# Kernel optimization log

Hardware: AMD Instinct MI355X
Metric: run time of the kernel (lower is better)

Reference implementation:

```python
import jax, jax.numpy as jnp
import numpy as np

B, T, D_FEAT, FREQ, HID = 256, 128, 128, 16, 128


def setup_inputs() -> dict:
    key = jax.random.key(0)
    ks = jax.random.split(key, 14)
    n = lambda k, s, sc: jax.random.normal(k, s, jnp.float32) * sc
    sx = float(np.sqrt(2.0 / (D_FEAT + HID)))   # xavier-ish for W_*
    sf = float(np.sqrt(2.0 / (D_FEAT + FREQ)))
    sh = float(np.sqrt(1.0 / HID))              # stand-in for orthogonal U_*
    return {
        "input": jax.random.normal(ks[0], (B, D_FEAT * T), jnp.float32),
        "W_i": n(ks[1], (D_FEAT, HID), sx), "U_i": n(ks[2], (HID, HID), sh), "b_i": jnp.zeros((HID,), jnp.float32),
        "W_ste": n(ks[3], (D_FEAT, HID), sx), "U_ste": n(ks[4], (HID, HID), sh), "b_ste": jnp.ones((HID,), jnp.float32),
        "W_fre": n(ks[5], (D_FEAT, FREQ), sf), "U_fre": n(ks[6], (HID, FREQ), sh), "b_fre": jnp.ones((FREQ,), jnp.float32),
        "W_c": n(ks[7], (D_FEAT, HID), sx), "U_c": n(ks[8], (HID, HID), sh), "b_c": jnp.zeros((HID,), jnp.float32),
        "W_o": n(ks[9], (D_FEAT, HID), sx), "U_o": n(ks[10], (HID, HID), sh), "b_o": jnp.zeros((HID,), jnp.float32),
        "U_a": n(ks[11], (FREQ, 1), sh), "b_a": jnp.zeros((HID,), jnp.float32),
        "W_sym": n(ks[12], (HID, 1), sh), "b_sym": jnp.zeros((1,), jnp.float32),
    }


def _hsig(z):  # torch.nn.Hardsigmoid: relu6(x+3)/6
    return jnp.clip(z / 6.0 + 0.5, 0.0, 1.0)


def reference(input, W_i, U_i, b_i, W_ste, U_ste, b_ste, W_fre, U_fre, b_fre,
              W_c, U_c, b_c, W_o, U_o, b_o, U_a, b_a, W_sym, b_sym):
    Bsz = input.shape[0]
    x = input.reshape(Bsz, D_FEAT, -1).transpose(0, 2, 1)  # (B, T, D)
    # hoist the 5 input projections out of the time loop (identical math)
    xi = jnp.einsum('btd,dh->tbh', x, W_i) + b_i
    xste = jnp.einsum('btd,dh->tbh', x, W_ste) + b_ste
    xfre = jnp.einsum('btd,df->tbf', x, W_fre) + b_fre
    xc = jnp.einsum('btd,dh->tbh', x, W_c) + b_c
    xo = jnp.einsum('btd,dh->tbh', x, W_o) + b_o
    frequency = jnp.arange(FREQ, dtype=jnp.float32) / FREQ
    two_pi = jnp.float32(2.0 * np.pi)
    ua = U_a[:, 0]  # (FREQ,)

    def step(carry, xs):
        h, S_re, S_im, t = carry
        xi_t, xste_t, xfre_t, xc_t, xo_t = xs
        i = _hsig(xi_t + h @ U_i)
        ste = _hsig(xste_t + h @ U_ste)
        fre = _hsig(xfre_t + h @ U_fre)
        f = ste[:, :, None] * fre[:, None, :]          # (B, H, F)
        c = i * jnp.tanh(xc_t + h @ U_c)               # (B, H)
        t = t + 1.0
        omega = two_pi * t * frequency                 # (F,)
        S_re = f * S_re + c[:, :, None] * jnp.cos(omega)
        S_im = f * S_im + c[:, :, None] * jnp.sin(omega)
        A = S_re * S_re + S_im * S_im                  # (B, H, F)
        a = jnp.tanh(jnp.einsum('bhf,f->bh', A, ua) + b_a)
        o = _hsig(xo_t + h @ U_o)
        h = o * a
        return (h, S_re, S_im, t), None

    init = (jnp.zeros((Bsz, HID), jnp.float32),
            jnp.zeros((Bsz, HID, FREQ), jnp.float32),
            jnp.zeros((Bsz, HID, FREQ), jnp.float32),
            jnp.float32(0.0))
    (h, _, _, _), _ = jax.lax.scan(step, init, (xi, xste, xfre, xc, xo))
    return h @ W_sym + b_sym  # (B, num_symbols)
```

## Files before the change

### kernel.cpp

```cpp
#include <hip/hip_runtime.h>
#include <hip/hip_bf16.h>
#include <hip/hip_fp16.h>


__device__ __forceinline__ float hsig_f(float z) {
    return fminf(fmaxf(z * (1.0f / 6.0f) + 0.5f, 0.0f), 1.0f);
}

__global__ __launch_bounds__(256) void proj_gemm(
    const float* __restrict__ input,
    const float* __restrict__ Wi, const float* __restrict__ Wste,
    const float* __restrict__ Wc, const float* __restrict__ Wo,
    const float* __restrict__ Wfre,
    const float* __restrict__ bi, const float* __restrict__ bste,
    const float* __restrict__ bc, const float* __restrict__ bo,
    const float* __restrict__ bfre,
    float* __restrict__ P)
{
    __shared__ __align__(16) float XT[128 * 64];
    __shared__ __align__(16) float WT[128 * 66];

    const int br  = blockIdx.x;
    const int b   = br >> 1;
    const int t0g = (br & 1) * 64;
    const int tid = threadIdx.x;

    const float* xb = input + (size_t)b * 16384 + t0g;
#pragma unroll
    for (int i = 0; i < 8; i++) {
        int f = (i * 256 + tid) * 4;
        int k = f >> 6, t = f & 63;
        *(float4*)(&XT[k * 64 + t]) = *(const float4*)(xb + k * 128 + t);
    }

    const int tx = tid & 31;
    const int ty = tid >> 5;

    const float* Ws[5]     = {Wi, Wste, Wc, Wo, Wfre};
    const float* biases[5] = {bi, bste, bc, bo, bfre};

    for (int ct = 0; ct < 5; ct++) {
        const float* W     = Ws[ct];
        const float* bias  = biases[ct];
        const int    ncols = (ct < 4) ? 128 : 16;
        const int    npass = (ct < 4) ? 2 : 1;
        const int    cbase = (ct < 4) ? ct * 128 : 512;

        for (int ch = 0; ch < npass; ch++) {
            __syncthreads();
#pragma unroll
            for (int i = 0; i < 8; i++) {
                int f = (i * 256 + tid) * 4;
                int k = f >> 6, c = f & 63;
                int gc = ch * 64 + c;
                if (gc < ncols)
                    *(float4*)(&WT[k * 66 + c]) = *(const float4*)(W + k * ncols + gc);
            }
            __syncthreads();

            float acc[8][2] = {};
#pragma unroll 4
            for (int k = 0; k < 128; k++) {
                float2 w  = *(const float2*)(&WT[k * 66 + tx * 2]);
                float4 x0 = *(const float4*)(&XT[k * 64 + ty * 8]);
                float4 x1 = *(const float4*)(&XT[k * 64 + ty * 8 + 4]);
                const float xr[8] = {x0.x, x0.y, x0.z, x0.w, x1.x, x1.y, x1.z, x1.w};
#pragma unroll
                for (int r = 0; r < 8; r++) {
                    acc[r][0] = fmaf(xr[r], w.x, acc[r][0]);
                    acc[r][1] = fmaf(xr[r], w.y, acc[r][1]);
                }
            }

            const int colg = ch * 64 + tx * 2;
            if (colg < ncols) {
                float b0 = bias[colg], b1 = bias[colg + 1];
#pragma unroll
                for (int r = 0; r < 8; r++) {
                    int row = br * 64 + ty * 8 + r;
                    float2 o = make_float2(acc[r][0] + b0, acc[r][1] + b1);
                    *(float2*)(&P[(size_t)row * 528 + cbase + colg]) = o;
                }
            }
        }
    }
}

__global__ __launch_bounds__(1024) void recur_kernel(
    const float* __restrict__ P,
    const float* __restrict__ Ui, const float* __restrict__ Uste,
    const float* __restrict__ Uc, const float* __restrict__ Uo,
    const float* __restrict__ Ufre,
    const float* __restrict__ Ua, const float* __restrict__ ba_g,
    const float* __restrict__ Wsym, const float* __restrict__ bsym,
    float* __restrict__ out)
{
    __shared__ __half2 u16_lds[4 * 64 * 128];
    __shared__ float ufre_t[16 * 132];
    __shared__ float costab[16], sintab[16];
    __shared__ float gate_buf[512];
    __shared__ float partial_buf[512];
    __shared__ float fre_buf[16];
    __shared__ float h_buf[128];

    const int tid  = threadIdx.x;
    const int lane = tid & 63;
    const int half = tid >> 9;
    const int c    = tid & 511;
    const int m    = c >> 7;
    const int j    = c & 127;
    const int hh   = tid >> 3;
    const int fsel = tid & 7;
    const int b    = blockIdx.x;

    for (int e = tid; e < 4 * 64 * 128; e += 1024) {
        int m_ = e >> 13, rem = e & 8191, kk = rem >> 7, jj = rem & 127;
        const float* Um = (m_ == 0) ? Ui : (m_ == 1) ? Uste : (m_ == 2) ? Uc : Uo;
        float lo = Um[(2 * kk) * 128 + jj];
        float hi = Um[(2 * kk + 1) * 128 + jj];
        u16_lds[e] = __floats2half2_rn(lo, hi);
    }
    for (int e = tid; e < 2048; e += 1024) {
        int k = e >> 4, col = e & 15;
        ufre_t[col * 132 + k] = Ufre[e];
    }
    if (tid < 16) {
        float ang = 6.283185307179586f * (float)tid * (1.0f / 16.0f);
        costab[tid] = cosf(ang);
        sintab[tid] = sinf(ang);
    }
    if (tid < 128) h_buf[tid] = 0.0f;

    const float ua0 = Ua[fsel];
    const float ua1 = Ua[fsel + 8];
    const float ba  = ba_g[hh];

    float hA = 0.0f;
    float Sre0 = 0.f, Sim0 = 0.f, Sre1 = 0.f, Sim1 = 0.f;
    int idx0 = 0, idx1 = 0;

    __syncthreads();

    const __half2* ucol = &u16_lds[(m << 13) + (half << 12) + j];

    const float* pr = P + (size_t)b * 128 * 528;
    for (int t = 0; t < 128; t++) {
        const float xpre = (half == 0) ? pr[c] : pr[512 + (c >> 5)];

        float a0 = 0.f, a1 = 0.f;
#pragma unroll
        for (int kk = 0; kk < 32; kk++) {
            __half2 uh = ucol[kk << 7];
            float s0 = __uint_as_float(__builtin_amdgcn_readlane(__float_as_uint(hA), 2 * kk));
            float s1 = __uint_as_float(__builtin_amdgcn_readlane(__float_as_uint(hA), 2 * kk + 1));
            a0 = fmaf(__low2float(uh),  s0, a0);
            a1 = fmaf(__high2float(uh), s1, a1);
        }
        float acc = a0 + a1;

        if (half) partial_buf[c] = acc;
        __syncthreads();

        if (half == 0) {
            float z = acc + partial_buf[c] + xpre;
            float g = (m == 2) ? tanhf(z) : hsig_f(z);
            gate_buf[c] = g;
        } else {
            const int col = c >> 5, kg = c & 31;
            float4 hv = *(const float4*)(&h_buf[kg * 4]);
            float4 uv = *(const float4*)(&ufre_t[col * 132 + kg * 4]);
            float p = fmaf(hv.x, uv.x, fmaf(hv.y, uv.y, fmaf(hv.z, uv.z, hv.w * uv.w)));
#pragma unroll
            for (int off = 1; off <= 16; off <<= 1) p += __shfl_xor(p, off, 64);
            if (kg == 0) fre_buf[col] = hsig_f(p + xpre);
        }
        __syncthreads();

        {
            float iv = gate_buf[hh];
            float sv = gate_buf[128 + hh];
            float tc = gate_buf[256 + hh];
            float ov = gate_buf[384 + hh];
            float cg = iv * tc;

            idx0 = (idx0 + fsel) & 15;
            idx1 = (idx1 + fsel + 8) & 15;

            float f0v = sv * fre_buf[fsel];
            float f1v = sv * fre_buf[fsel + 8];
            Sre0 = fmaf(f0v, Sre0, cg * costab[idx0]);
            Sim0 = fmaf(f0v, Sim0, cg * sintab[idx0]);
            Sre1 = fmaf(f1v, Sre1, cg * costab[idx1]);
            Sim1 = fmaf(f1v, Sim1, cg * sintab[idx1]);

            float aacc = fmaf(Sre0, Sre0, Sim0 * Sim0) * ua0;
            aacc = fmaf(fmaf(Sre1, Sre1, Sim1 * Sim1), ua1, aacc);
            aacc += __shfl_xor(aacc, 1, 64);
            aacc += __shfl_xor(aacc, 2, 64);
            aacc += __shfl_xor(aacc, 4, 64);
            if (fsel == 0) {
                float a = tanhf(aacc + ba);
                h_buf[hh] = ov * a;
            }
        }
        __syncthreads();
        hA = h_buf[half * 64 + lane];
        pr += 528;
    }

    if (tid < 64) {
        float v = fmaf(h_buf[lane], Wsym[lane], h_buf[64 + lane] * Wsym[64 + lane]);
#pragma unroll
        for (int off = 1; off <= 32; off <<= 1) v += __shfl_xor(v, off, 64);
        if (lane == 0) out[b] = v + bsym[0];
    }
}

extern "C" void kernel_launch(void* const* d_in, const int* in_sizes, int n_in,
                              void* d_out, int out_size, void* d_ws, size_t ws_size,
                              hipStream_t stream) {
    const float* input = (const float*)d_in[0];
    const float* W_i   = (const float*)d_in[1];
    const float* U_i   = (const float*)d_in[2];
    const float* b_i   = (const float*)d_in[3];
    const float* W_ste = (const float*)d_in[4];
    const float* U_ste = (const float*)d_in[5];
    const float* b_ste = (const float*)d_in[6];
    const float* W_fre = (const float*)d_in[7];
    const float* U_fre = (const float*)d_in[8];
    const float* b_fre = (const float*)d_in[9];
    const float* W_c   = (const float*)d_in[10];
    const float* U_c   = (const float*)d_in[11];
    const float* b_c   = (const float*)d_in[12];
    const float* W_o   = (const float*)d_in[13];
    const float* U_o   = (const float*)d_in[14];
    const float* b_o   = (const float*)d_in[15];
    const float* U_a   = (const float*)d_in[16];
    const float* b_a   = (const float*)d_in[17];
    const float* W_sym = (const float*)d_in[18];
    const float* b_sym = (const float*)d_in[19];

    float* P = (float*)d_ws;

    proj_gemm<<<512, 256, 0, stream>>>(
        input, W_i, W_ste, W_c, W_o, W_fre,
        b_i, b_ste, b_c, b_o, b_fre, P);

    recur_kernel<<<256, 1024, 0, stream>>>(
        P, U_i, U_ste, U_c, U_o, U_fre,
        U_a, b_a, W_sym, b_sym, (float*)d_out);
}
```

Measured before the change: 429.5 us.

## Use packed fp16 dot2 on half-precision h and drop split-K partial sync

```diff
diff --git a/kernel.cpp b/kernel.cpp
--- a/kernel.cpp
+++ b/kernel.cpp
@@ -2,6 +2,21 @@
 #include <hip/hip_bf16.h>
 #include <hip/hip_fp16.h>
 
+
+typedef _Float16 h2t __attribute__((ext_vector_type(2)));
+
+__device__ __forceinline__ h2t bch(unsigned int v) {
+    union { unsigned int u; h2t h; } c; c.u = v; return c.h;
+}
+__device__ __forceinline__ float dot2f(unsigned int u, unsigned int h, float acc) {
+#if __has_builtin(__builtin_amdgcn_fdot2)
+    return __builtin_amdgcn_fdot2(bch(u), bch(h), acc, false);
+#else
+    h2t a = bch(u), b = bch(h);
+    acc = fmaf((float)a[0], (float)b[0], acc);
+    return fmaf((float)a[1], (float)b[1], acc);
+#endif
+}
 
 __device__ __forceinline__ float hsig_f(float z) {
     return fminf(fmaxf(z * (1.0f / 6.0f) + 0.5f, 0.0f), 1.0f);
@@ -95,30 +110,33 @@
     const float* __restrict__ Wsym, const float* __restrict__ bsym,
     float* __restrict__ out)
 {
-    __shared__ __half2 u16_lds[4 * 64 * 128];
-    __shared__ float ufre_t[16 * 132];
+    __shared__ __align__(16) unsigned int u_lds[4 * 64 * 128];
+    __shared__ __align__(16) float ufre_t[16 * 132];
+    __shared__ __align__(16) __half h16[128];
     __shared__ float costab[16], sintab[16];
     __shared__ float gate_buf[512];
-    __shared__ float partial_buf[512];
     __shared__ float fre_buf[16];
     __shared__ float h_buf[128];
 
     const int tid  = threadIdx.x;
-    const int lane = tid & 63;
-    const int half = tid >> 9;
-    const int c    = tid & 511;
-    const int m    = c >> 7;
-    const int j    = c & 127;
+    const int b    = blockIdx.x;
     const int hh   = tid >> 3;
     const int fsel = tid & 7;
-    const int b    = blockIdx.x;
+
+    const bool is_col = (tid < 512);
+    const int  c   = tid & 511;
+    const int  m   = c >> 7;
+    const int  j   = c & 127;
+    const int  fcol = c >> 5;
+    const int  kg   = c & 31;
 
     for (int e = tid; e < 4 * 64 * 128; e += 1024) {
         int m_ = e >> 13, rem = e & 8191, kk = rem >> 7, jj = rem & 127;
         const float* Um = (m_ == 0) ? Ui : (m_ == 1) ? Uste : (m_ == 2) ? Uc : Uo;
-        float lo = Um[(2 * kk) * 128 + jj];
-        float hi = Um[(2 * kk + 1) * 128 + jj];
-        u16_lds[e] = __floats2half2_rn(lo, hi);
+        union { h2t h; unsigned int u; } p;
+        p.h[0] = (_Float16)Um[(2 * kk) * 128 + jj];
+        p.h[1] = (_Float16)Um[(2 * kk + 1) * 128 + jj];
+        u_lds[e] = p.u;
     }
     for (int e = tid; e < 2048; e += 1024) {
         int k = e >> 4, col = e & 15;
@@ -129,50 +147,48 @@
         costab[tid] = cosf(ang);
         sintab[tid] = sinf(ang);
     }
-    if (tid < 128) h_buf[tid] = 0.0f;
+    if (tid < 128) { h_buf[tid] = 0.0f; h16[tid] = __float2half(0.0f); }
 
     const float ua0 = Ua[fsel];
     const float ua1 = Ua[fsel + 8];
     const float ba  = ba_g[hh];
 
-    float hA = 0.0f;
     float Sre0 = 0.f, Sim0 = 0.f, Sre1 = 0.f, Sim1 = 0.f;
     int idx0 = 0, idx1 = 0;
 
     __syncthreads();
 
-    const __half2* ucol = &u16_lds[(m << 13) + (half << 12) + j];
+    const unsigned int* ucol = u_lds + (m << 13) + j;
+    const uint4* h4 = (const uint4*)h16;
 
     const float* pr = P + (size_t)b * 128 * 528;
     for (int t = 0; t < 128; t++) {
-        const float xpre = (half == 0) ? pr[c] : pr[512 + (c >> 5)];
-
-        float a0 = 0.f, a1 = 0.f;
-#pragma unroll
-        for (int kk = 0; kk < 32; kk++) {
-            __half2 uh = ucol[kk << 7];
-            float s0 = __uint_as_float(__builtin_amdgcn_readlane(__float_as_uint(hA), 2 * kk));
-            float s1 = __uint_as_float(__builtin_amdgcn_readlane(__float_as_uint(hA), 2 * kk + 1));
-            a0 = fmaf(__low2float(uh),  s0, a0);
-            a1 = fmaf(__high2float(uh), s1, a1);
-        }
-        float acc = a0 + a1;
-
-        if (half) partial_buf[c] = acc;
-        __syncthreads();
-
-        if (half == 0) {
-            float z = acc + partial_buf[c] + xpre;
+        if (is_col) {
+            const float xpre = pr[c];
+            float a0 = 0.f, a1 = 0.f, a2 = 0.f, a3 = 0.f;
+#pragma unroll
+            for (int q = 0; q < 16; q++) {
+                uint4 hv = h4[q];
+                unsigned int u0 = ucol[(4 * q + 0) << 7];
+                unsigned int u1 = ucol[(4 * q + 1) << 7];
+                unsigned int u2 = ucol[(4 * q + 2) << 7];
+                unsigned int u3 = ucol[(4 * q + 3) << 7];
+                a0 = dot2f(u0, hv.x, a0);
+                a1 = dot2f(u1, hv.y, a1);
+                a2 = dot2f(u2, hv.z, a2);
+                a3 = dot2f(u3, hv.w, a3);
+            }
+            float z = (a0 + a1) + (a2 + a3) + xpre;
             float g = (m == 2) ? tanhf(z) : hsig_f(z);
             gate_buf[c] = g;
         } else {
-            const int col = c >> 5, kg = c & 31;
+            const float xfre = pr[512 + fcol];
             float4 hv = *(const float4*)(&h_buf[kg * 4]);
-            float4 uv = *(const float4*)(&ufre_t[col * 132 + kg * 4]);
+            float4 uv = *(const float4*)(&ufre_t[fcol * 132 + kg * 4]);
             float p = fmaf(hv.x, uv.x, fmaf(hv.y, uv.y, fmaf(hv.z, uv.z, hv.w * uv.w)));
 #pragma unroll
             for (int off = 1; off <= 16; off <<= 1) p += __shfl_xor(p, off, 64);
-            if (kg == 0) fre_buf[col] = hsig_f(p + xpre);
+            if (kg == 0) fre_buf[fcol] = hsig_f(p + xfre);
         }
         __syncthreads();
 
@@ -199,20 +215,21 @@
             aacc += __shfl_xor(aacc, 2, 64);
             aacc += __shfl_xor(aacc, 4, 64);
             if (fsel == 0) {
-                float a = tanhf(aacc + ba);
-                h_buf[hh] = ov * a;
+                float a  = tanhf(aacc + ba);
+                float hv = ov * a;
+                h_buf[hh] = hv;
+                h16[hh]   = __float2half(hv);
             }
         }
         __syncthreads();
-        hA = h_buf[half * 64 + lane];
         pr += 528;
     }
 
     if (tid < 64) {
-        float v = fmaf(h_buf[lane], Wsym[lane], h_buf[64 + lane] * Wsym[64 + lane]);
+        float v = fmaf(h_buf[tid], Wsym[tid], h_buf[64 + tid] * Wsym[64 + tid]);
 #pragma unroll
         for (int off = 1; off <= 32; off <<= 1) v += __shfl_xor(v, off, 64);
-        if (lane == 0) out[b] = v + bsym[0];
+        if (tid == 0) out[b] = v + bsym[0];
     }
 }
 
```

After: 363.8 us. -15.3%, faster.
